# Kernel optimization log

Measured on AMD Instinct MI355X. Metric: run time of the kernel, lower is better.

The kernel has to match this reference:

```python
import jax, jax.numpy as jnp
import numpy as np
import math

_INV_SQRT2 = 1.0 / math.sqrt(2.0)
B, N, D, H = 4, 8192, 1024, 16
DH = D // H  # 64
GH = 4 * DH  # 256


def setup_inputs() -> dict:
    key = jax.random.key(0)
    ks = jax.random.split(key, 8)
    std = 0.02
    return {
        "x": jax.random.normal(ks[0], (B, N, D), jnp.float32),
        "w_q": jax.random.normal(ks[1], (D, D), jnp.float32) * std,
        "w_v": jax.random.normal(ks[2], (D, D), jnp.float32) * std,
        "w_o": jax.random.normal(ks[3], (D, D), jnp.float32) * std,
        "ln_g": jnp.ones((DH,), jnp.float32),
        "ln_b": jnp.zeros((DH,), jnp.float32),
        "gate_w1": jax.random.normal(ks[4], (DH, GH), jnp.float32) * std,
        "gate_w2": jax.random.normal(ks[5], (GH, 2 * N), jnp.float32) * std,
        "wrm_w1": jax.random.normal(ks[6], (DH, GH), jnp.float32) * std,
        "wrm_w2": jax.random.normal(ks[7], (GH, N), jnp.float32) * std,
    }


def reference(x, w_q, w_v, w_o, ln_g, ln_b, gate_w1, gate_w2, wrm_w1, wrm_w2):
    b, n, d = x.shape
    h, dh = H, DH
    # projections -> (b, h, n, dh)
    q = (x @ w_q).reshape(b, n, h, dh).transpose(0, 2, 1, 3)
    v = (x @ w_v).reshape(b, n, h, dh).transpose(0, 2, 1, 3)
    # per-head summary query + LayerNorm (biased variance, eps=1e-5)
    bar_q = q.mean(axis=2)  # (b, h, dh)
    mu = bar_q.mean(axis=-1, keepdims=True)
    var = ((bar_q - mu) ** 2).mean(axis=-1, keepdims=True)
    bar_q = (bar_q - mu) / jnp.sqrt(var + 1e-5) * ln_g + ln_b
    # complex spectral gate: (b, h, 2n) -> real || imag
    g_raw = jax.nn.gelu(bar_q @ gate_w1, approximate=False) @ gate_w2
    g = g_raw[..., :n] + 1j * g_raw[..., n:]  # (b, h, n) complex
    # FFT -> gate -> IFFT along sequence axis
    v_hat = jnp.fft.fft(v, axis=2) * g[..., None]
    v_tilde = jnp.fft.ifft(v_hat, axis=2).real.astype(x.dtype)
    # Haar wavelet refinement
    even, odd = v_tilde[..., 0::2, :], v_tilde[..., 1::2, :]
    w_hat = jnp.concatenate([(even + odd) * _INV_SQRT2,
                             (even - odd) * _INV_SQRT2], axis=-2)
    s = (jax.nn.gelu(bar_q @ wrm_w1, approximate=False) @ wrm_w2)[..., None]
    w_hat = w_hat * s
    half = n // 2
    low, high = w_hat[..., :half, :], w_hat[..., half:, :]
    ev = (low + high) * _INV_SQRT2
    od = (low - high) * _INV_SQRT2
    v_ref = jnp.stack([ev, od], axis=-2).reshape(b, h, n, dh)  # interleave even/odd
    v_tilde = v_tilde + v_ref
    y = v_tilde.transpose(0, 2, 1, 3).reshape(b, n, d)
    return y @ w_o
```

## Files before the change

kernel.cpp:

```cpp
#include <hip/hip_runtime.h>
#include <hip/hip_bf16.h>
#include <math.h>

#define PB 4
#define PN 8192
#define PD 1024
#define PH 16
#define PDH 64
#define PGH 256

typedef __bf16 bf16x8 __attribute__((ext_vector_type(8)));
typedef __bf16 bf16x2 __attribute__((ext_vector_type(2)));
typedef float f32x4 __attribute__((ext_vector_type(4)));
typedef unsigned int u32;
typedef unsigned short u16;

typedef __attribute__((address_space(3))) void lds_void_t;
typedef const __attribute__((address_space(1))) void gbl_void_t;
#define ASYNC_COPY16(gp, lp) \
    __builtin_amdgcn_global_load_lds((gbl_void_t*)(gp), (lds_void_t*)(lp), 16, 0, 0)

__device__ inline float gelu_exact(float x) {
    return 0.5f * x * (1.0f + erff(x * 0.70710678118654752440f));
}

__device__ inline float2 f2(float x, float y) { return make_float2(x, y); }
__device__ inline float2 cadd(float2 a, float2 b) { return f2(a.x + b.x, a.y + b.y); }
__device__ inline float2 csub(float2 a, float2 b) { return f2(a.x - b.x, a.y - b.y); }
__device__ inline float2 cmul(float2 a, float2 b) {
    return f2(a.x * b.x - a.y * b.y, a.x * b.y + a.y * b.x);
}

#define PHYS(i) ((i) ^ (((i) >> 4) & 15))

__device__ inline u32 packbf(float a, float b) {
    __bf16 ba = (__bf16)a, bb = (__bf16)b;
    return (u32)(*(u16*)&ba) | ((u32)(*(u16*)&bb) << 16);
}

__global__ void convert_x(const float* __restrict__ x, __bf16* __restrict__ xb) {
    int i = (blockIdx.x * 256 + threadIdx.x) * 8;
    float4 f0 = *(const float4*)(x + i);
    float4 f1 = *(const float4*)(x + i + 4);
    bf16x8 o;
    o[0] = (__bf16)f0.x; o[1] = (__bf16)f0.y; o[2] = (__bf16)f0.z; o[3] = (__bf16)f0.w;
    o[4] = (__bf16)f1.x; o[5] = (__bf16)f1.y; o[6] = (__bf16)f1.z; o[7] = (__bf16)f1.w;
    *(bf16x8*)(xb + i) = o;
}

__global__ void transpose_w(const float* __restrict__ wv, const float* __restrict__ wo,
                            __bf16* __restrict__ wvt, __bf16* __restrict__ wot) {
    int idx = blockIdx.x * 256 + threadIdx.x;
    const float* src = blockIdx.y ? wo : wv;
    __bf16* dst = blockIdx.y ? wot : wvt;
    int r = idx >> 10, c = idx & 1023;
    dst[c * PD + r] = (__bf16)src[idx];
}

__global__ void reduce_x(const float* __restrict__ x, float* __restrict__ xsum) {
    int b = blockIdx.z;
    int d = blockIdx.y * 256 + threadIdx.x;
    int n0 = blockIdx.x * 512;
    const float* p = x + ((size_t)b * PN + n0) * PD + d;
    float s = 0.0f;
    for (int i = 0; i < 512; i++) s += p[(size_t)i * PD];
    atomicAdd(&xsum[b * PD + d], s);
}

__global__ void barq_ln(const float* __restrict__ xsum, const float* __restrict__ w_q,
                        const float* __restrict__ ln_g, const float* __restrict__ ln_b,
                        float* __restrict__ bar_ln) {
    int b = blockIdx.y;
    int c = blockIdx.x * 256 + threadIdx.x;
    const float* xs = xsum + b * PD;
    float acc = 0.0f;
    for (int k = 0; k < PD; k++) acc += xs[k] * w_q[k * PD + c];
    float bar = acc * (1.0f / (float)PN);
    float mu = bar;
    for (int o = 32; o > 0; o >>= 1) mu += __shfl_xor(mu, o, 64);
    mu *= (1.0f / 64.0f);
    float d0 = bar - mu;
    float vv = d0 * d0;
    for (int o = 32; o > 0; o >>= 1) vv += __shfl_xor(vv, o, 64);
    vv *= (1.0f / 64.0f);
    int dh = c & 63;
    bar_ln[b * PD + c] = d0 * rsqrtf(vv + 1e-5f) * ln_g[dh] + ln_b[dh];
}

__global__ void small1(const float* __restrict__ bar_ln, const float* __restrict__ gw1,
                       const float* __restrict__ ww1, float* __restrict__ tg,
                       float* __restrict__ tw) {
    int bh = blockIdx.x;
    int j = threadIdx.x;
    __shared__ float bl[PDH];
    if (j < PDH) bl[j] = bar_ln[bh * PDH + j];
    __syncthreads();
    float a1 = 0.0f, a2 = 0.0f;
    for (int k = 0; k < PDH; k++) {
        float bv = bl[k];
        a1 += bv * gw1[k * PGH + j];
        a2 += bv * ww1[k * PGH + j];
    }
    tg[bh * PGH + j] = gelu_exact(a1);
    tw[bh * PGH + j] = gelu_exact(a2);
}

__global__ void small2(const float* __restrict__ tg, const float* __restrict__ tw,
                       const float* __restrict__ gw2, const float* __restrict__ ww2,
                       float* __restrict__ g_raw, float* __restrict__ s_full) {
    int chunk = blockIdx.x;
    int bh0 = blockIdx.y * 8;
    bool isg = chunk < 64;
    const float* t = isg ? tg : tw;
    const float* w2 = isg ? gw2 : ww2;
    int stride = isg ? (2 * PN) : PN;
    int col = (isg ? chunk : chunk - 64) * 256 + threadIdx.x;
    __shared__ float tl[8][PGH];
    #pragma unroll
    for (int i = 0; i < 8; i++) tl[i][threadIdx.x] = t[(bh0 + i) * PGH + threadIdx.x];
    __syncthreads();
    float acc[8] = {0, 0, 0, 0, 0, 0, 0, 0};
    for (int k = 0; k < PGH; k++) {
        float w = w2[(size_t)k * stride + col];
        #pragma unroll
        for (int i = 0; i < 8; i++) acc[i] += tl[i][k] * w;
    }
    #pragma unroll
    for (int i = 0; i < 8; i++) {
        if (isg) g_raw[(size_t)(bh0 + i) * (2 * PN) + col] = acc[i];
        else     s_full[(size_t)(bh0 + i) * PN + col] = acc[i];
    }
}

__global__ __launch_bounds__(256) void gemm_pair(const __bf16* __restrict__ A,
                                                 const __bf16* __restrict__ Bt,
                                                 u32* __restrict__ vt) {
    constexpr int K = PD, LDK = 32;
    __shared__ __attribute__((aligned(16))) __bf16 As[128 * LDK];
    __shared__ __attribute__((aligned(16))) __bf16 Bs[128 * LDK];
    const int tid = threadIdx.x;
    const int lane = tid & 63;
    const int wave = tid >> 6;
    const int wm = (wave >> 1) << 6;
    const int wn = (wave & 1) << 6;
    const int tileM = blockIdx.y << 7;
    const int tileN = blockIdx.x << 7;
    const int r = tid >> 2;
    const int cg = tid & 3;
    const int mrow = lane & 15;
    const int k0 = (lane >> 4) << 3;

    f32x4 acc[4][4] = {};
    const __bf16* Aptr = A + (size_t)(tileM + r) * K + cg * 8;
    const __bf16* Bptr = Bt + (size_t)(tileN + r) * K + cg * 8;

    for (int kt = 0; kt < K; kt += 32) {
        __syncthreads();
        ASYNC_COPY16(Aptr + kt,                  As + tid * 8);
        ASYNC_COPY16(Aptr + (size_t)64 * K + kt, As + 64 * LDK + tid * 8);
        ASYNC_COPY16(Bptr + kt,                  Bs + tid * 8);
        ASYNC_COPY16(Bptr + (size_t)64 * K + kt, Bs + 64 * LDK + tid * 8);
        __syncthreads();
        bf16x8 af[4], bfr[4];
        #pragma unroll
        for (int i = 0; i < 4; i++) af[i]  = *(const bf16x8*)&As[(wm + i * 16 + mrow) * LDK + k0];
        #pragma unroll
        for (int j = 0; j < 4; j++) bfr[j] = *(const bf16x8*)&Bs[(wn + j * 16 + mrow) * LDK + k0];
        #pragma unroll
        for (int i = 0; i < 4; i++)
            #pragma unroll
            for (int j = 0; j < 4; j++)
                acc[i][j] = __builtin_amdgcn_mfma_f32_16x16x32_bf16(af[i], bfr[j], acc[i][j], 0, 0, 0);
    }

    const int rq = (lane >> 4) << 2;
    const bool evl = (lane & 1) == 0;
    #pragma unroll
    for (int i = 0; i < 4; i++) {
        int grow = tileM + wm + i * 16 + rq;
        int b = grow >> 13;
        int nb = grow & 8191;
        #pragma unroll
        for (int j = 0; j < 4; j++) {
            u32 w[4];
            #pragma unroll
            for (int rr = 0; rr < 4; rr++) {
                float a = acc[i][j][rr];
                float o = __shfl_xor(a, 1, 64);
                w[rr] = packbf(a, o);
            }
            if (evl) {
                int col = tileN + wn + j * 16 + mrow;
                size_t idx = ((size_t)b * 512 + (col >> 1)) * PN + nb;
                *(uint4*)(vt + idx) = make_uint4(w[0], w[1], w[2], w[3]);
            }
        }
    }
}

__global__ __launch_bounds__(256) void gemm_ta(const u32* __restrict__ yt,
                                               const __bf16* __restrict__ Bt,
                                               float* __restrict__ Cf) {
    constexpr int K = PD, Nc = PD, LDKA = 40, LDKB = 32;
    __shared__ __attribute__((aligned(16))) __bf16 As[128 * LDKA];
    __shared__ __attribute__((aligned(16))) __bf16 Bs[128 * LDKB];
    u32* As32 = (u32*)As;
    const int tid = threadIdx.x;
    const int lane = tid & 63;
    const int wave = tid >> 6;
    const int wm = (wave >> 1) << 6;
    const int wn = (wave & 1) << 6;
    const int tileM = blockIdx.y << 7;
    const int tileN = blockIdx.x << 7;
    const int r = tid >> 2;
    const int cg = tid & 3;
    const int mrow = lane & 15;
    const int k0 = (lane >> 4) << 3;
    const int prow = tid & 7;
    const int seg = tid >> 3;

    const int b = tileM >> 13;
    const int n0 = tileM & 8191;
    const u32* abase = yt + ((size_t)b * 512 + prow) * PN + n0 + seg * 4;
    const __bf16* Bptr = Bt + (size_t)(tileN + r) * K + cg * 8;

    f32x4 acc[4][4] = {};
    uint4 pa0 = *(const uint4*)(abase);
    uint4 pa1 = *(const uint4*)(abase + (size_t)8 * PN);

    for (int kt = 0; kt < K; kt += 32) {
        __syncthreads();
        {
            int m0 = seg * 4;
            As32[(m0 + 0) * 20 + prow] = pa0.x;
            As32[(m0 + 1) * 20 + prow] = pa0.y;
            As32[(m0 + 2) * 20 + prow] = pa0.z;
            As32[(m0 + 3) * 20 + prow] = pa0.w;
            As32[(m0 + 0) * 20 + prow + 8] = pa1.x;
            As32[(m0 + 1) * 20 + prow + 8] = pa1.y;
            As32[(m0 + 2) * 20 + prow + 8] = pa1.z;
            As32[(m0 + 3) * 20 + prow + 8] = pa1.w;
        }
        ASYNC_COPY16(Bptr + kt,                  Bs + tid * 8);
        ASYNC_COPY16(Bptr + (size_t)64 * K + kt, Bs + 64 * LDKB + tid * 8);
        if (kt + 32 < K) {
            const u32* nxt = abase + (size_t)((kt >> 1) + 16) * PN;
            pa0 = *(const uint4*)(nxt);
            pa1 = *(const uint4*)(nxt + (size_t)8 * PN);
        }
        __syncthreads();
        bf16x8 af[4], bfr[4];
        #pragma unroll
        for (int i = 0; i < 4; i++) af[i]  = *(const bf16x8*)&As[(wm + i * 16 + mrow) * LDKA + k0];
        #pragma unroll
        for (int j = 0; j < 4; j++) bfr[j] = *(const bf16x8*)&Bs[(wn + j * 16 + mrow) * LDKB + k0];
        #pragma unroll
        for (int i = 0; i < 4; i++)
            #pragma unroll
            for (int j = 0; j < 4; j++)
                acc[i][j] = __builtin_amdgcn_mfma_f32_16x16x32_bf16(af[i], bfr[j], acc[i][j], 0, 0, 0);
    }

    const int rq = (lane >> 4) << 2;
    #pragma unroll
    for (int i = 0; i < 4; i++) {
        #pragma unroll
        for (int rr = 0; rr < 4; rr++) {
            int row = tileM + wm + i * 16 + rq + rr;
            size_t base = (size_t)row * Nc + tileN + wn + mrow;
            #pragma unroll
            for (int j = 0; j < 4; j++) Cf[base + j * 16] = acc[i][j][rr];
        }
    }
}

__global__ __launch_bounds__(512) void fftconv(const u32* __restrict__ vt,
                                               const float* __restrict__ g_raw,
                                               const float* __restrict__ s_full,
                                               u32* __restrict__ yt) {
    __shared__ float2 Z[PN];
    const int tid = threadIdx.x;
    const int row = blockIdx.x;
    const int bh = row >> 5;
    const u32* vp = vt + (size_t)row * PN;

    #pragma unroll
    for (int it = 0; it < 2; it++) {
        int n0 = (tid + it * 512) * 8;
        uint4 u0 = *(const uint4*)(vp + n0);
        uint4 u1 = *(const uint4*)(vp + n0 + 4);
        u32 uu[8] = {u0.x, u0.y, u0.z, u0.w, u1.x, u1.y, u1.z, u1.w};
        #pragma unroll
        for (int m = 0; m < 8; m++) {
            bf16x2 p = *(bf16x2*)&uu[m];
            Z[PHYS(n0 + m)] = f2((float)p.x, (float)p.y);
        }
    }
    __syncthreads();

    #pragma unroll
    for (int si = 0; si < 6; si++) {
        const int s = 11 - 2 * si;
        const int h = 1 << s;
        const float ang = -6.283185307179586f / (float)(4 * h);
        float sn, cs;
        __sincosf(ang * (float)(tid & (h - 1)), &sn, &cs);
        float2 w2 = f2(cs, sn);
        #pragma unroll
        for (int it = 0; it < 4; it++) {
            int q = tid + it * 512;
            int i = ((q >> s) << (s + 2)) + (q & (h - 1));
            float2 w1 = cmul(w2, w2);
            float2 a = Z[PHYS(i)],         bb = Z[PHYS(i + h)];
            float2 c = Z[PHYS(i + 2 * h)], d  = Z[PHYS(i + 3 * h)];
            float2 A0 = cadd(a, c);
            float2 C0 = cmul(csub(a, c), w2);
            float2 B0 = cadd(bb, d);
            float2 t  = cmul(csub(bb, d), w2);
            float2 D0 = f2(t.y, -t.x);
            Z[PHYS(i)]         = cadd(A0, B0);
            Z[PHYS(i + h)]     = cmul(csub(A0, B0), w1);
            Z[PHYS(i + 2 * h)] = cadd(C0, D0);
            Z[PHYS(i + 3 * h)] = cmul(csub(C0, D0), w1);
            if (h == 2048) w2 = cmul(w2, f2(0.92387953251f, -0.38268343236f));
        }
        __syncthreads();
    }
    #pragma unroll
    for (int it = 0; it < 8; it++) {
        int i = 2 * (tid + it * 512);
        float2 u = Z[PHYS(i)], t = Z[PHYS(i + 1)];
        Z[PHYS(i)]     = cadd(u, t);
        Z[PHYS(i + 1)] = csub(u, t);
    }
    __syncthreads();

    const float* gr = g_raw + (size_t)bh * (2 * PN);
    const float* gi = gr + PN;
    for (int m = tid; m < PN / 2 + 1; m += 512) {
        int p  = (m < PN / 2) ? 2 * m : 1;
        int k  = __brev((unsigned)p) >> 19;
        int Nk = (PN - k) & (PN - 1);
        int qd = __brev((unsigned)Nk) >> 19;
        float2 Za = Z[PHYS(p)], Zb = Z[PHYS(qd)];
        float v1r = 0.5f * (Za.x + Zb.x), v1i = 0.5f * (Za.y - Zb.y);
        float v2r = 0.5f * (Za.y + Zb.y), v2i = 0.5f * (Zb.x - Za.x);
        float grk = gr[k],  gik = gi[k];
        float grn = gr[Nk], gin = gi[Nk];
        float y1r  = v1r * grk - v1i * gik, y1i  = v1r * gik + v1i * grk;
        float y2r  = v2r * grk - v2i * gik, y2i  = v2r * gik + v2i * grk;
        float y1nr = v1r * grn + v1i * gin, y1ni = v1r * gin - v1i * grn;
        float y2nr = v2r * grn + v2i * gin, y2ni = v2r * gin - v2i * grn;
        float ys1r = 0.5f * (y1r + y1nr), ys1i = 0.5f * (y1i - y1ni);
        float ys2r = 0.5f * (y2r + y2nr), ys2i = 0.5f * (y2i - y2ni);
        Z[PHYS(p)] = f2(ys1r - ys2i, ys1i + ys2r);
        if (qd != p) Z[PHYS(qd)] = f2(ys1r + ys2i, ys2r - ys1i);
    }
    __syncthreads();

    #pragma unroll
    for (int si = 0; si < 6; si++) {
        const int s = 2 * si;
        const int h = 1 << s;
        const float ang = 6.283185307179586f / (float)(4 * h);
        float sn, cs;
        __sincosf(ang * (float)(tid & (h - 1)), &sn, &cs);
        float2 w2a = f2(cs, sn);
        float2 w2b = (h == 1024) ? cmul(w2a, f2(0.70710678119f, 0.70710678119f)) : w2a;
        #pragma unroll
        for (int it = 0; it < 4; it++) {
            int q = tid + it * 512;
            int i = ((q >> s) << (s + 2)) + (q & (h - 1));
            float2 w2 = (it & 1) ? w2b : w2a;
            float2 w1 = cmul(w2, w2);
            float2 a = Z[PHYS(i)],         bb = Z[PHYS(i + h)];
            float2 c = Z[PHYS(i + 2 * h)], d  = Z[PHYS(i + 3 * h)];
            float2 tb = cmul(bb, w1);
            float2 p0 = cadd(a, tb), p1 = csub(a, tb);
            float2 td = cmul(d, w1);
            float2 q0 = cadd(c, td), q1 = csub(c, td);
            float2 wq0 = cmul(q0, w2);
            float2 e   = cmul(q1, w2);
            float2 ei  = f2(-e.y, e.x);
            Z[PHYS(i)]         = cadd(p0, wq0);
            Z[PHYS(i + 2 * h)] = csub(p0, wq0);
            Z[PHYS(i + h)]     = cadd(p1, ei);
            Z[PHYS(i + 3 * h)] = csub(p1, ei);
        }
        __syncthreads();
    }
    {
        const float ang = 6.283185307179586f / (float)PN;
        float sn, cs;
        __sincosf(ang * (float)tid, &sn, &cs);
        float2 w = f2(cs, sn);
        #pragma unroll
        for (int it = 0; it < 8; it++) {
            int q = tid + it * 512;
            float2 u = Z[PHYS(q)];
            float2 t = cmul(Z[PHYS(q + PN / 2)], w);
            Z[PHYS(q)]          = cadd(u, t);
            Z[PHYS(q + PN / 2)] = csub(u, t);
            w = cmul(w, f2(0.92387953251f, 0.38268343236f));
        }
    }
    __syncthreads();

    const float* sp = s_full + (size_t)bh * PN;
    u32* yp = yt + (size_t)row * PN;
    const float inv = 1.0f / (float)PN;
    const float I2 = 0.70710678118654752440f;
    #pragma unroll
    for (int it = 0; it < 2; it++) {
        int nb = tid + it * 512;
        int n0 = nb * 8;
        int np0 = nb * 4;
        u32 ou[8];
        #pragma unroll
        for (int pp = 0; pp < 4; pp++) {
            float2 z0 = Z[PHYS(n0 + 2 * pp)];
            float2 z1 = Z[PHYS(n0 + 2 * pp + 1)];
            float s0  = sp[np0 + pp];
            float s1v = sp[np0 + pp + PN / 2];
            float ax = z0.x * inv, ay = z0.y * inv;
            float bx = z1.x * inv, by = z1.y * inv;
            float wlx = (ax + bx) * I2 * s0, whx = (ax - bx) * I2 * s1v;
            float evx = (wlx + whx) * I2,   odx = (wlx - whx) * I2;
            float wly = (ay + by) * I2 * s0, why = (ay - by) * I2 * s1v;
            float evy = (wly + why) * I2,   ody = (wly - why) * I2;
            ou[2 * pp]     = packbf(ax + evx, ay + evy);
            ou[2 * pp + 1] = packbf(bx + odx, by + ody);
        }
        *(uint4*)(yp + n0)     = make_uint4(ou[0], ou[1], ou[2], ou[3]);
        *(uint4*)(yp + n0 + 4) = make_uint4(ou[4], ou[5], ou[6], ou[7]);
    }
}

extern "C" void kernel_launch(void* const* d_in, const int* in_sizes, int n_in,
                              void* d_out, int out_size, void* d_ws, size_t ws_size,
                              hipStream_t stream) {
    const float* x    = (const float*)d_in[0];
    const float* w_q  = (const float*)d_in[1];
    const float* w_v  = (const float*)d_in[2];
    const float* w_o  = (const float*)d_in[3];
    const float* ln_g = (const float*)d_in[4];
    const float* ln_b = (const float*)d_in[5];
    const float* gw1  = (const float*)d_in[6];
    const float* gw2  = (const float*)d_in[7];
    const float* ww1  = (const float*)d_in[8];
    const float* ww2  = (const float*)d_in[9];
    float* out = (float*)d_out;

    const size_t XE = (size_t)PB * PN * PD;
    __bf16* xb   = (__bf16*)d_ws;
    __bf16* vb   = xb + XE;
    __bf16* wvt  = vb + XE;
    __bf16* wot  = wvt + (size_t)PD * PD;
    float*  xsum = (float*)(wot + (size_t)PD * PD);
    float*  bar  = xsum + PB * PD;
    float*  tg   = bar + PB * PD;
    float*  tw   = tg + 64 * PGH;
    float*  graw = tw + 64 * PGH;
    float*  sful = graw + (size_t)64 * 2 * PN;

    hipMemsetAsync(xsum, 0, PB * PD * sizeof(float), stream);

    convert_x<<<XE / (256 * 8), 256, 0, stream>>>(x, xb);
    transpose_w<<<dim3(PD * PD / 256, 2), 256, 0, stream>>>(w_v, w_o, wvt, wot);
    reduce_x<<<dim3(PN / 512, PD / 256, PB), 256, 0, stream>>>(x, xsum);
    barq_ln<<<dim3(PD / 256, PB), 256, 0, stream>>>(xsum, w_q, ln_g, ln_b, bar);
    small1<<<PB * PH, 256, 0, stream>>>(bar, gw1, ww1, tg, tw);
    small2<<<dim3(96, 8), 256, 0, stream>>>(tg, tw, gw2, ww2, graw, sful);
    gemm_pair<<<dim3(PD / 128, PB * PN / 128), 256, 0, stream>>>(xb, wvt, (u32*)vb);
    fftconv<<<PB * 512, 512, 0, stream>>>((const u32*)vb, graw, sful, (u32*)xb);
    gemm_ta<<<dim3(PD / 128, PB * PN / 128), 256, 0, stream>>>((const u32*)xb, wot, out);
}
```

Before: 779.1 us.

## Fuse x conversion with reduction, tile weight transpose, register-blocked radix-16 FFT

Result: faster. 724.8 us (-7.0%).

```diff
diff --git a/kernel.cpp b/kernel.cpp
--- a/kernel.cpp
+++ b/kernel.cpp
@@ -38,53 +38,150 @@
     return (u32)(*(u16*)&ba) | ((u32)(*(u16*)&bb) << 16);
 }
 
-__global__ void convert_x(const float* __restrict__ x, __bf16* __restrict__ xb) {
-    int i = (blockIdx.x * 256 + threadIdx.x) * 8;
-    float4 f0 = *(const float4*)(x + i);
-    float4 f1 = *(const float4*)(x + i + 4);
-    bf16x8 o;
-    o[0] = (__bf16)f0.x; o[1] = (__bf16)f0.y; o[2] = (__bf16)f0.z; o[3] = (__bf16)f0.w;
-    o[4] = (__bf16)f1.x; o[5] = (__bf16)f1.y; o[6] = (__bf16)f1.z; o[7] = (__bf16)f1.w;
-    *(bf16x8*)(xb + i) = o;
+__device__ inline void dif4(float2& a, float2& b, float2& c, float2& d,
+                            float2 w2, float2 w1) {
+    float2 A0 = cadd(a, c);
+    float2 C0 = cmul(csub(a, c), w2);
+    float2 B0 = cadd(b, d);
+    float2 t  = cmul(csub(b, d), w2);
+    float2 D0 = f2(t.y, -t.x);
+    a = cadd(A0, B0);
+    b = cmul(csub(A0, B0), w1);
+    c = cadd(C0, D0);
+    d = cmul(csub(C0, D0), w1);
+}
+
+__device__ inline void dit4(float2& a, float2& b, float2& c, float2& d,
+                            float2 w2, float2 w1) {
+    float2 tb = cmul(b, w1);
+    float2 p0 = cadd(a, tb), p1 = csub(a, tb);
+    float2 td = cmul(d, w1);
+    float2 q0 = cadd(c, td), q1 = csub(c, td);
+    float2 wq0 = cmul(q0, w2);
+    float2 e   = cmul(q1, w2);
+    float2 ei  = f2(-e.y, e.x);
+    a = cadd(p0, wq0);
+    c = csub(p0, wq0);
+    b = cadd(p1, ei);
+    d = csub(p1, ei);
+}
+
+template<int S>
+__device__ inline void fwd16_layers(float2 X[4][4], int u) {
+    const int h4 = 1 << (S - 2);
+    const int off = u & (h4 - 1);
+    float sn, cs;
+    const float ang1 = -6.283185307179586f / (float)(1 << (S + 2));
+    __sincosf(ang1 * (float)off, &sn, &cs);
+    float2 w2 = f2(cs, sn);
+    const float2 c8m = f2(0.92387953251129f, -0.38268343236509f);
+    #pragma unroll
+    for (int b = 0; b < 4; b++) {
+        float2 w1 = cmul(w2, w2);
+        dif4(X[0][b], X[1][b], X[2][b], X[3][b], w2, w1);
+        w2 = cmul(w2, c8m);
+    }
+    const float ang2 = -6.283185307179586f / (float)(1 << S);
+    __sincosf(ang2 * (float)off, &sn, &cs);
+    float2 v2 = f2(cs, sn);
+    float2 v1 = cmul(v2, v2);
+    #pragma unroll
+    for (int a = 0; a < 4; a++)
+        dif4(X[a][0], X[a][1], X[a][2], X[a][3], v2, v1);
+}
+
+template<int S>
+__device__ inline void inv16_layers(float2 X[4][4], int u) {
+    const int h = 1 << S;
+    const int off = u & (h - 1);
+    float sn, cs;
+    const float ang1 = 6.283185307179586f / (float)(4 * h);
+    __sincosf(ang1 * (float)off, &sn, &cs);
+    float2 w2 = f2(cs, sn), w1 = cmul(w2, w2);
+    #pragma unroll
+    for (int a = 0; a < 4; a++)
+        dit4(X[a][0], X[a][1], X[a][2], X[a][3], w2, w1);
+    const float ang2 = 6.283185307179586f / (float)(16 * h);
+    __sincosf(ang2 * (float)off, &sn, &cs);
+    float2 v2 = f2(cs, sn);
+    const float2 c8p = f2(0.92387953251129f, 0.38268343236509f);
+    #pragma unroll
+    for (int b = 0; b < 4; b++) {
+        float2 v1 = cmul(v2, v2);
+        dit4(X[0][b], X[1][b], X[2][b], X[3][b], v2, v1);
+        v2 = cmul(v2, c8p);
+    }
+}
+
+__device__ inline void r2_shfl(float2 X[4][4], bool ev) {
+    #pragma unroll
+    for (int a = 0; a < 4; a++)
+        #pragma unroll
+        for (int b = 0; b < 4; b++) {
+            float2 o = f2(__shfl_xor(X[a][b].x, 1, 64), __shfl_xor(X[a][b].y, 1, 64));
+            X[a][b] = ev ? cadd(X[a][b], o) : csub(o, X[a][b]);
+        }
+}
+
+__global__ void convert_reduce(const float* __restrict__ x, __bf16* __restrict__ xb,
+                               float* __restrict__ xsum) {
+    int b = blockIdx.z;
+    int d = blockIdx.y * 256 + threadIdx.x;
+    int n0 = blockIdx.x * 256;
+    const float* p = x + ((size_t)b * PN + n0) * PD + d;
+    __bf16* q = xb + ((size_t)b * PN + n0) * PD + d;
+    float s = 0.0f;
+    #pragma unroll 4
+    for (int i = 0; i < 256; i++) {
+        float v = p[(size_t)i * PD];
+        s += v;
+        q[(size_t)i * PD] = (__bf16)v;
+    }
+    atomicAdd(&xsum[b * PD + d], s);
 }
 
 __global__ void transpose_w(const float* __restrict__ wv, const float* __restrict__ wo,
                             __bf16* __restrict__ wvt, __bf16* __restrict__ wot) {
-    int idx = blockIdx.x * 256 + threadIdx.x;
-    const float* src = blockIdx.y ? wo : wv;
-    __bf16* dst = blockIdx.y ? wot : wvt;
-    int r = idx >> 10, c = idx & 1023;
-    dst[c * PD + r] = (__bf16)src[idx];
-}
-
-__global__ void reduce_x(const float* __restrict__ x, float* __restrict__ xsum) {
-    int b = blockIdx.z;
-    int d = blockIdx.y * 256 + threadIdx.x;
-    int n0 = blockIdx.x * 512;
-    const float* p = x + ((size_t)b * PN + n0) * PD + d;
-    float s = 0.0f;
-    for (int i = 0; i < 512; i++) s += p[(size_t)i * PD];
-    atomicAdd(&xsum[b * PD + d], s);
+    __shared__ float t[64][65];
+    const float* src = blockIdx.z ? wo : wv;
+    __bf16* dst = blockIdx.z ? wot : wvt;
+    int r0 = blockIdx.y * 64, c0 = blockIdx.x * 64;
+    int lr = threadIdx.x >> 6, lc = threadIdx.x & 63;
+    #pragma unroll
+    for (int i = 0; i < 16; i++)
+        t[lr + 4 * i][lc] = src[(size_t)(r0 + lr + 4 * i) * PD + c0 + lc];
+    __syncthreads();
+    #pragma unroll
+    for (int i = 0; i < 16; i++)
+        dst[(size_t)(c0 + lr + 4 * i) * PD + r0 + lc] = (__bf16)t[lc][lr + 4 * i];
 }
 
 __global__ void barq_ln(const float* __restrict__ xsum, const float* __restrict__ w_q,
                         const float* __restrict__ ln_g, const float* __restrict__ ln_b,
                         float* __restrict__ bar_ln) {
     int b = blockIdx.y;
-    int c = blockIdx.x * 256 + threadIdx.x;
-    const float* xs = xsum + b * PD;
+    int lane = threadIdx.x & 63;
+    int w = threadIdx.x >> 6;
+    int c = blockIdx.x * 64 + lane;
+    const float* xs = xsum + b * PD + w * 256;
+    const float* wq = w_q + (size_t)(w * 256) * PD + c;
     float acc = 0.0f;
-    for (int k = 0; k < PD; k++) acc += xs[k] * w_q[k * PD + c];
-    float bar = acc * (1.0f / (float)PN);
-    float mu = bar;
-    for (int o = 32; o > 0; o >>= 1) mu += __shfl_xor(mu, o, 64);
-    mu *= (1.0f / 64.0f);
-    float d0 = bar - mu;
-    float vv = d0 * d0;
-    for (int o = 32; o > 0; o >>= 1) vv += __shfl_xor(vv, o, 64);
-    vv *= (1.0f / 64.0f);
-    int dh = c & 63;
-    bar_ln[b * PD + c] = d0 * rsqrtf(vv + 1e-5f) * ln_g[dh] + ln_b[dh];
+    for (int k = 0; k < 256; k++) acc += xs[k] * wq[(size_t)k * PD];
+    __shared__ float part[4][64];
+    part[w][lane] = acc;
+    __syncthreads();
+    if (w == 0) {
+        float bar = (part[0][lane] + part[1][lane] + part[2][lane] + part[3][lane])
+                    * (1.0f / (float)PN);
+        float mu = bar;
+        for (int o = 32; o > 0; o >>= 1) mu += __shfl_xor(mu, o, 64);
+        mu *= (1.0f / 64.0f);
+        float d0 = bar - mu;
+        float vv = d0 * d0;
+        for (int o = 32; o > 0; o >>= 1) vv += __shfl_xor(vv, o, 64);
+        vv *= (1.0f / 64.0f);
+        bar_ln[b * PD + c] = d0 * rsqrtf(vv + 1e-5f) * ln_g[lane] + ln_b[lane];
+    }
 }
 
 __global__ void small1(const float* __restrict__ bar_ln, const float* __restrict__ gw1,
@@ -283,156 +380,167 @@
     const int row = blockIdx.x;
     const int bh = row >> 5;
     const u32* vp = vt + (size_t)row * PN;
-
-    #pragma unroll
-    for (int it = 0; it < 2; it++) {
-        int n0 = (tid + it * 512) * 8;
-        uint4 u0 = *(const uint4*)(vp + n0);
-        uint4 u1 = *(const uint4*)(vp + n0 + 4);
-        u32 uu[8] = {u0.x, u0.y, u0.z, u0.w, u1.x, u1.y, u1.z, u1.w};
-        #pragma unroll
-        for (int m = 0; m < 8; m++) {
-            bf16x2 p = *(bf16x2*)&uu[m];
-            Z[PHYS(n0 + m)] = f2((float)p.x, (float)p.y);
-        }
-    }
-    __syncthreads();
-
-    #pragma unroll
-    for (int si = 0; si < 6; si++) {
-        const int s = 11 - 2 * si;
-        const int h = 1 << s;
-        const float ang = -6.283185307179586f / (float)(4 * h);
-        float sn, cs;
-        __sincosf(ang * (float)(tid & (h - 1)), &sn, &cs);
-        float2 w2 = f2(cs, sn);
-        #pragma unroll
-        for (int it = 0; it < 4; it++) {
-            int q = tid + it * 512;
-            int i = ((q >> s) << (s + 2)) + (q & (h - 1));
-            float2 w1 = cmul(w2, w2);
-            float2 a = Z[PHYS(i)],         bb = Z[PHYS(i + h)];
-            float2 c = Z[PHYS(i + 2 * h)], d  = Z[PHYS(i + 3 * h)];
-            float2 A0 = cadd(a, c);
-            float2 C0 = cmul(csub(a, c), w2);
-            float2 B0 = cadd(bb, d);
-            float2 t  = cmul(csub(bb, d), w2);
-            float2 D0 = f2(t.y, -t.x);
-            Z[PHYS(i)]         = cadd(A0, B0);
-            Z[PHYS(i + h)]     = cmul(csub(A0, B0), w1);
-            Z[PHYS(i + 2 * h)] = cadd(C0, D0);
-            Z[PHYS(i + 3 * h)] = cmul(csub(C0, D0), w1);
-            if (h == 2048) w2 = cmul(w2, f2(0.92387953251f, -0.38268343236f));
-        }
-        __syncthreads();
-    }
-    #pragma unroll
-    for (int it = 0; it < 8; it++) {
-        int i = 2 * (tid + it * 512);
-        float2 u = Z[PHYS(i)], t = Z[PHYS(i + 1)];
-        Z[PHYS(i)]     = cadd(u, t);
-        Z[PHYS(i + 1)] = csub(u, t);
-    }
-    __syncthreads();
-
-    const float* gr = g_raw + (size_t)bh * (2 * PN);
-    const float* gi = gr + PN;
-    for (int m = tid; m < PN / 2 + 1; m += 512) {
-        int p  = (m < PN / 2) ? 2 * m : 1;
-        int k  = __brev((unsigned)p) >> 19;
-        int Nk = (PN - k) & (PN - 1);
-        int qd = __brev((unsigned)Nk) >> 19;
-        float2 Za = Z[PHYS(p)], Zb = Z[PHYS(qd)];
-        float v1r = 0.5f * (Za.x + Zb.x), v1i = 0.5f * (Za.y - Zb.y);
-        float v2r = 0.5f * (Za.y + Zb.y), v2i = 0.5f * (Zb.x - Za.x);
-        float grk = gr[k],  gik = gi[k];
-        float grn = gr[Nk], gin = gi[Nk];
-        float y1r  = v1r * grk - v1i * gik, y1i  = v1r * gik + v1i * grk;
-        float y2r  = v2r * grk - v2i * gik, y2i  = v2r * gik + v2i * grk;
-        float y1nr = v1r * grn + v1i * gin, y1ni = v1r * gin - v1i * grn;
-        float y2nr = v2r * grn + v2i * gin, y2ni = v2r * gin - v2i * grn;
-        float ys1r = 0.5f * (y1r + y1nr), ys1i = 0.5f * (y1i - y1ni);
-        float ys2r = 0.5f * (y2r + y2nr), ys2i = 0.5f * (y2i - y2ni);
-        Z[PHYS(p)] = f2(ys1r - ys2i, ys1i + ys2r);
-        if (qd != p) Z[PHYS(qd)] = f2(ys1r + ys2i, ys2r - ys1i);
-    }
-    __syncthreads();
-
-    #pragma unroll
-    for (int si = 0; si < 6; si++) {
-        const int s = 2 * si;
-        const int h = 1 << s;
-        const float ang = 6.283185307179586f / (float)(4 * h);
-        float sn, cs;
-        __sincosf(ang * (float)(tid & (h - 1)), &sn, &cs);
-        float2 w2a = f2(cs, sn);
-        float2 w2b = (h == 1024) ? cmul(w2a, f2(0.70710678119f, 0.70710678119f)) : w2a;
-        #pragma unroll
-        for (int it = 0; it < 4; it++) {
-            int q = tid + it * 512;
-            int i = ((q >> s) << (s + 2)) + (q & (h - 1));
-            float2 w2 = (it & 1) ? w2b : w2a;
-            float2 w1 = cmul(w2, w2);
-            float2 a = Z[PHYS(i)],         bb = Z[PHYS(i + h)];
-            float2 c = Z[PHYS(i + 2 * h)], d  = Z[PHYS(i + 3 * h)];
-            float2 tb = cmul(bb, w1);
-            float2 p0 = cadd(a, tb), p1 = csub(a, tb);
-            float2 td = cmul(d, w1);
-            float2 q0 = cadd(c, td), q1 = csub(c, td);
-            float2 wq0 = cmul(q0, w2);
-            float2 e   = cmul(q1, w2);
-            float2 ei  = f2(-e.y, e.x);
-            Z[PHYS(i)]         = cadd(p0, wq0);
-            Z[PHYS(i + 2 * h)] = csub(p0, wq0);
-            Z[PHYS(i + h)]     = cadd(p1, ei);
-            Z[PHYS(i + 3 * h)] = csub(p1, ei);
-        }
-        __syncthreads();
-    }
-    {
-        const float ang = 6.283185307179586f / (float)PN;
-        float sn, cs;
-        __sincosf(ang * (float)tid, &sn, &cs);
-        float2 w = f2(cs, sn);
-        #pragma unroll
-        for (int it = 0; it < 8; it++) {
-            int q = tid + it * 512;
-            float2 u = Z[PHYS(q)];
-            float2 t = cmul(Z[PHYS(q + PN / 2)], w);
-            Z[PHYS(q)]          = cadd(u, t);
-            Z[PHYS(q + PN / 2)] = csub(u, t);
-            w = cmul(w, f2(0.92387953251f, 0.38268343236f));
-        }
-    }
-    __syncthreads();
-
-    const float* sp = s_full + (size_t)bh * PN;
-    u32* yp = yt + (size_t)row * PN;
-    const float inv = 1.0f / (float)PN;
-    const float I2 = 0.70710678118654752440f;
-    #pragma unroll
-    for (int it = 0; it < 2; it++) {
-        int nb = tid + it * 512;
-        int n0 = nb * 8;
-        int np0 = nb * 4;
-        u32 ou[8];
-        #pragma unroll
-        for (int pp = 0; pp < 4; pp++) {
-            float2 z0 = Z[PHYS(n0 + 2 * pp)];
-            float2 z1 = Z[PHYS(n0 + 2 * pp + 1)];
-            float s0  = sp[np0 + pp];
-            float s1v = sp[np0 + pp + PN / 2];
-            float ax = z0.x * inv, ay = z0.y * inv;
-            float bx = z1.x * inv, by = z1.y * inv;
-            float wlx = (ax + bx) * I2 * s0, whx = (ax - bx) * I2 * s1v;
-            float evx = (wlx + whx) * I2,   odx = (wlx - whx) * I2;
-            float wly = (ay + by) * I2 * s0, why = (ay - by) * I2 * s1v;
-            float evy = (wly + why) * I2,   ody = (wly - why) * I2;
-            ou[2 * pp]     = packbf(ax + evx, ay + evy);
-            ou[2 * pp + 1] = packbf(bx + odx, by + ody);
-        }
-        *(uint4*)(yp + n0)     = make_uint4(ou[0], ou[1], ou[2], ou[3]);
-        *(uint4*)(yp + n0 + 4) = make_uint4(ou[4], ou[5], ou[6], ou[7]);
+    const bool ev = (tid & 1) == 0;
+
+    {
+        float2 X[4][4];
+        #pragma unroll
+        for (int a = 0; a < 4; a++)
+            #pragma unroll
+            for (int b = 0; b < 4; b++) {
+                u32 pw = vp[tid + a * 2048 + b * 512];
+                bf16x2 pp = *(bf16x2*)&pw;
+                X[a][b] = f2((float)pp.x, (float)pp.y);
+            }
+        fwd16_layers<11>(X, tid);
+        #pragma unroll
+        for (int a = 0; a < 4; a++)
+            #pragma unroll
+            for (int b = 0; b < 4; b++)
+                Z[PHYS(tid + a * 2048 + b * 512)] = X[a][b];
+    }
+    __syncthreads();
+
+    {
+        const int base = ((tid >> 5) << 9) + (tid & 31);
+        float2 X[4][4];
+        #pragma unroll
+        for (int a = 0; a < 4; a++)
+            #pragma unroll
+            for (int b = 0; b < 4; b++)
+                X[a][b] = Z[PHYS(base + a * 128 + b * 32)];
+        fwd16_layers<7>(X, tid);
+        #pragma unroll
+        for (int a = 0; a < 4; a++)
+            #pragma unroll
+            for (int b = 0; b < 4; b++)
+                Z[PHYS(base + a * 128 + b * 32)] = X[a][b];
+    }
+    __syncthreads();
+
+    {
+        const int base = ((tid >> 1) << 5) + (tid & 1);
+        float2 X[4][4];
+        #pragma unroll
+        for (int a = 0; a < 4; a++)
+            #pragma unroll
+            for (int b = 0; b < 4; b++)
+                X[a][b] = Z[PHYS(base + a * 8 + b * 2)];
+        fwd16_layers<3>(X, tid);
+        r2_shfl(X, ev);
+        #pragma unroll
+        for (int a = 0; a < 4; a++)
+            #pragma unroll
+            for (int b = 0; b < 4; b++)
+                Z[PHYS(base + a * 8 + b * 2)] = X[a][b];
+    }
+    __syncthreads();
+
+    {
+        const float* gr = g_raw + (size_t)bh * (2 * PN);
+        const float* gi = gr + PN;
+        for (int m = tid; m < PN / 2 + 1; m += 512) {
+            int p  = (m < PN / 2) ? 2 * m : 1;
+            int k  = __brev((unsigned)p) >> 19;
+            int Nk = (PN - k) & (PN - 1);
+            int qd = __brev((unsigned)Nk) >> 19;
+            float2 Za = Z[PHYS(p)], Zb = Z[PHYS(qd)];
+            float v1r = 0.5f * (Za.x + Zb.x), v1i = 0.5f * (Za.y - Zb.y);
+            float v2r = 0.5f * (Za.y + Zb.y), v2i = 0.5f * (Zb.x - Za.x);
+            float grk = gr[k],  gik = gi[k];
+            float grn = gr[Nk], gin = gi[Nk];
+            float y1r  = v1r * grk - v1i * gik, y1i  = v1r * gik + v1i * grk;
+            float y2r  = v2r * grk - v2i * gik, y2i  = v2r * gik + v2i * grk;
+            float y1nr = v1r * grn + v1i * gin, y1ni = v1r * gin - v1i * grn;
+            float y2nr = v2r * grn + v2i * gin, y2ni = v2r * gin - v2i * grn;
+            float ys1r = 0.5f * (y1r + y1nr), ys1i = 0.5f * (y1i - y1ni);
+            float ys2r = 0.5f * (y2r + y2nr), ys2i = 0.5f * (y2i - y2ni);
+            Z[PHYS(p)] = f2(ys1r - ys2i, ys1i + ys2r);
+            if (qd != p) Z[PHYS(qd)] = f2(ys1r + ys2i, ys2r - ys1i);
+        }
+    }
+    __syncthreads();
+
+    {
+        const int base = ((tid >> 1) << 5) + (tid & 1);
+        float2 X[4][4];
+        #pragma unroll
+        for (int a = 0; a < 4; a++)
+            #pragma unroll
+            for (int b = 0; b < 4; b++)
+                X[a][b] = Z[PHYS(base + a * 8 + b * 2)];
+        r2_shfl(X, ev);
+        inv16_layers<1>(X, tid);
+        #pragma unroll
+        for (int a = 0; a < 4; a++)
+            #pragma unroll
+            for (int b = 0; b < 4; b++)
+                Z[PHYS(base + a * 8 + b * 2)] = X[a][b];
+    }
+    __syncthreads();
+
+    {
+        const int base = ((tid >> 5) << 9) + (tid & 31);
+        float2 X[4][4];
+        #pragma unroll
+        for (int a = 0; a < 4; a++)
+            #pragma unroll
+            for (int b = 0; b < 4; b++)
+                X[a][b] = Z[PHYS(base + a * 128 + b * 32)];
+        inv16_layers<5>(X, tid);
+        #pragma unroll
+        for (int a = 0; a < 4; a++)
+            #pragma unroll
+            for (int b = 0; b < 4; b++)
+                Z[PHYS(base + a * 128 + b * 32)] = X[a][b];
+    }
+    __syncthreads();
+
+    {
+        float2 X[4][4];
+        #pragma unroll
+        for (int a = 0; a < 4; a++)
+            #pragma unroll
+            for (int b = 0; b < 4; b++)
+                X[a][b] = Z[PHYS(tid + a * 2048 + b * 512)];
+        inv16_layers<9>(X, tid);
+        #pragma unroll
+        for (int a = 0; a < 4; a++)
+            #pragma unroll
+            for (int b = 0; b < 4; b++)
+                Z[PHYS(tid + a * 2048 + b * 512)] = X[a][b];
+    }
+    __syncthreads();
+
+    {
+        const float* sp = s_full + (size_t)bh * PN;
+        u32* yp = yt + (size_t)row * PN;
+        const float inv = 1.0f / (float)PN;
+        const float I2 = 0.70710678118654752440f;
+        #pragma unroll
+        for (int it = 0; it < 2; it++) {
+            int nb = tid + it * 512;
+            int n0 = nb * 8;
+            int np0 = nb * 4;
+            u32 ou[8];
+            #pragma unroll
+            for (int pp = 0; pp < 4; pp++) {
+                float2 z0 = Z[PHYS(n0 + 2 * pp)];
+                float2 z1 = Z[PHYS(n0 + 2 * pp + 1)];
+                float s0  = sp[np0 + pp];
+                float s1v = sp[np0 + pp + PN / 2];
+                float ax = z0.x * inv, ay = z0.y * inv;
+                float bx = z1.x * inv, by = z1.y * inv;
+                float wlx = (ax + bx) * I2 * s0, whx = (ax - bx) * I2 * s1v;
+                float evx = (wlx + whx) * I2,   odx = (wlx - whx) * I2;
+                float wly = (ay + by) * I2 * s0, why = (ay - by) * I2 * s1v;
+                float evy = (wly + why) * I2,   ody = (wly - why) * I2;
+                ou[2 * pp]     = packbf(ax + evx, ay + evy);
+                ou[2 * pp + 1] = packbf(bx + odx, by + ody);
+            }
+            *(uint4*)(yp + n0)     = make_uint4(ou[0], ou[1], ou[2], ou[3]);
+            *(uint4*)(yp + n0 + 4) = make_uint4(ou[4], ou[5], ou[6], ou[7]);
+        }
     }
 }
 
@@ -465,10 +573,9 @@
 
     hipMemsetAsync(xsum, 0, PB * PD * sizeof(float), stream);
 
-    convert_x<<<XE / (256 * 8), 256, 0, stream>>>(x, xb);
-    transpose_w<<<dim3(PD * PD / 256, 2), 256, 0, stream>>>(w_v, w_o, wvt, wot);
-    reduce_x<<<dim3(PN / 512, PD / 256, PB), 256, 0, stream>>>(x, xsum);
-    barq_ln<<<dim3(PD / 256, PB), 256, 0, stream>>>(xsum, w_q, ln_g, ln_b, bar);
+    convert_reduce<<<dim3(PN / 256, PD / 256, PB), 256, 0, stream>>>(x, xb, xsum);
+    transpose_w<<<dim3(16, 16, 2), 256, 0, stream>>>(w_v, w_o, wvt, wot);
+    barq_ln<<<dim3(PD / 64, PB), 256, 0, stream>>>(xsum, w_q, ln_g, ln_b, bar);
     small1<<<PB * PH, 256, 0, stream>>>(bar, gw1, ww1, tg, tw);
     small2<<<dim3(96, 8), 256, 0, stream>>>(tg, tw, gw2, ww2, graw, sful);
     gemm_pair<<<dim3(PD / 128, PB * PN / 128), 256, 0, stream>>>(xb, wvt, (u32*)vb);
```

## Fuse x conversion with column reduction, tile weight transpose, split barq, XCD-swizzle GEMMs

Applied to the files above, without the earlier changes.

Result: faster. 679.9 us (-12.7%).

```diff
diff --git a/kernel.cpp b/kernel.cpp
--- a/kernel.cpp
+++ b/kernel.cpp
@@ -38,53 +38,65 @@
     return (u32)(*(u16*)&ba) | ((u32)(*(u16*)&bb) << 16);
 }
 
-__global__ void convert_x(const float* __restrict__ x, __bf16* __restrict__ xb) {
-    int i = (blockIdx.x * 256 + threadIdx.x) * 8;
-    float4 f0 = *(const float4*)(x + i);
-    float4 f1 = *(const float4*)(x + i + 4);
-    bf16x8 o;
-    o[0] = (__bf16)f0.x; o[1] = (__bf16)f0.y; o[2] = (__bf16)f0.z; o[3] = (__bf16)f0.w;
-    o[4] = (__bf16)f1.x; o[5] = (__bf16)f1.y; o[6] = (__bf16)f1.z; o[7] = (__bf16)f1.w;
-    *(bf16x8*)(xb + i) = o;
+__global__ void convert_reduce(const float* __restrict__ x, __bf16* __restrict__ xb,
+                               float* __restrict__ xsum) {
+    int b = blockIdx.z;
+    int d = blockIdx.y * 256 + threadIdx.x;
+    int n0 = blockIdx.x * 256;
+    const float* p = x + ((size_t)b * PN + n0) * PD + d;
+    __bf16* q = xb + ((size_t)b * PN + n0) * PD + d;
+    float s = 0.0f;
+    #pragma unroll 4
+    for (int i = 0; i < 256; i++) {
+        float v = p[(size_t)i * PD];
+        s += v;
+        q[(size_t)i * PD] = (__bf16)v;
+    }
+    atomicAdd(&xsum[b * PD + d], s);
 }
 
 __global__ void transpose_w(const float* __restrict__ wv, const float* __restrict__ wo,
                             __bf16* __restrict__ wvt, __bf16* __restrict__ wot) {
-    int idx = blockIdx.x * 256 + threadIdx.x;
-    const float* src = blockIdx.y ? wo : wv;
-    __bf16* dst = blockIdx.y ? wot : wvt;
-    int r = idx >> 10, c = idx & 1023;
-    dst[c * PD + r] = (__bf16)src[idx];
-}
-
-__global__ void reduce_x(const float* __restrict__ x, float* __restrict__ xsum) {
-    int b = blockIdx.z;
-    int d = blockIdx.y * 256 + threadIdx.x;
-    int n0 = blockIdx.x * 512;
-    const float* p = x + ((size_t)b * PN + n0) * PD + d;
-    float s = 0.0f;
-    for (int i = 0; i < 512; i++) s += p[(size_t)i * PD];
-    atomicAdd(&xsum[b * PD + d], s);
+    __shared__ float t[64][65];
+    const float* src = blockIdx.z ? wo : wv;
+    __bf16* dst = blockIdx.z ? wot : wvt;
+    int r0 = blockIdx.y * 64, c0 = blockIdx.x * 64;
+    int lr = threadIdx.x >> 6, lc = threadIdx.x & 63;
+    #pragma unroll
+    for (int i = 0; i < 16; i++)
+        t[lr + 4 * i][lc] = src[(size_t)(r0 + lr + 4 * i) * PD + c0 + lc];
+    __syncthreads();
+    #pragma unroll
+    for (int i = 0; i < 16; i++)
+        dst[(size_t)(c0 + lr + 4 * i) * PD + r0 + lc] = (__bf16)t[lc][lr + 4 * i];
 }
 
 __global__ void barq_ln(const float* __restrict__ xsum, const float* __restrict__ w_q,
                         const float* __restrict__ ln_g, const float* __restrict__ ln_b,
                         float* __restrict__ bar_ln) {
     int b = blockIdx.y;
-    int c = blockIdx.x * 256 + threadIdx.x;
-    const float* xs = xsum + b * PD;
+    int lane = threadIdx.x & 63;
+    int w = threadIdx.x >> 6;
+    int c = blockIdx.x * 64 + lane;
+    const float* xs = xsum + b * PD + w * 256;
+    const float* wq = w_q + (size_t)(w * 256) * PD + c;
     float acc = 0.0f;
-    for (int k = 0; k < PD; k++) acc += xs[k] * w_q[k * PD + c];
-    float bar = acc * (1.0f / (float)PN);
-    float mu = bar;
-    for (int o = 32; o > 0; o >>= 1) mu += __shfl_xor(mu, o, 64);
-    mu *= (1.0f / 64.0f);
-    float d0 = bar - mu;
-    float vv = d0 * d0;
-    for (int o = 32; o > 0; o >>= 1) vv += __shfl_xor(vv, o, 64);
-    vv *= (1.0f / 64.0f);
-    int dh = c & 63;
-    bar_ln[b * PD + c] = d0 * rsqrtf(vv + 1e-5f) * ln_g[dh] + ln_b[dh];
+    for (int k = 0; k < 256; k++) acc += xs[k] * wq[(size_t)k * PD];
+    __shared__ float part[4][64];
+    part[w][lane] = acc;
+    __syncthreads();
+    if (w == 0) {
+        float bar = (part[0][lane] + part[1][lane] + part[2][lane] + part[3][lane])
+                    * (1.0f / (float)PN);
+        float mu = bar;
+        for (int o = 32; o > 0; o >>= 1) mu += __shfl_xor(mu, o, 64);
+        mu *= (1.0f / 64.0f);
+        float d0 = bar - mu;
+        float vv = d0 * d0;
+        for (int o = 32; o > 0; o >>= 1) vv += __shfl_xor(vv, o, 64);
+        vv *= (1.0f / 64.0f);
+        bar_ln[b * PD + c] = d0 * rsqrtf(vv + 1e-5f) * ln_g[lane] + ln_b[lane];
+    }
 }
 
 __global__ void small1(const float* __restrict__ bar_ln, const float* __restrict__ gw1,
@@ -132,6 +144,16 @@
     }
 }
 
+__device__ inline void xcd_swizzle(int& tileM, int& tileN) {
+    int lin = blockIdx.x + (blockIdx.y << 3);
+    int xcd = lin & 7;
+    int idx = lin >> 3;
+    int yy = (xcd << 5) + (idx >> 3);
+    int xx = idx & 7;
+    tileM = yy << 7;
+    tileN = xx << 7;
+}
+
 __global__ __launch_bounds__(256) void gemm_pair(const __bf16* __restrict__ A,
                                                  const __bf16* __restrict__ Bt,
                                                  u32* __restrict__ vt) {
@@ -143,8 +165,8 @@
     const int wave = tid >> 6;
     const int wm = (wave >> 1) << 6;
     const int wn = (wave & 1) << 6;
-    const int tileM = blockIdx.y << 7;
-    const int tileN = blockIdx.x << 7;
+    int tileM, tileN;
+    xcd_swizzle(tileM, tileN);
     const int r = tid >> 2;
     const int cg = tid & 3;
     const int mrow = lane & 15;
@@ -210,8 +232,8 @@
     const int wave = tid >> 6;
     const int wm = (wave >> 1) << 6;
     const int wn = (wave & 1) << 6;
-    const int tileM = blockIdx.y << 7;
-    const int tileN = blockIdx.x << 7;
+    int tileM, tileN;
+    xcd_swizzle(tileM, tileN);
     const int r = tid >> 2;
     const int cg = tid & 3;
     const int mrow = lane & 15;
@@ -465,10 +487,9 @@
 
     hipMemsetAsync(xsum, 0, PB * PD * sizeof(float), stream);
 
-    convert_x<<<XE / (256 * 8), 256, 0, stream>>>(x, xb);
-    transpose_w<<<dim3(PD * PD / 256, 2), 256, 0, stream>>>(w_v, w_o, wvt, wot);
-    reduce_x<<<dim3(PN / 512, PD / 256, PB), 256, 0, stream>>>(x, xsum);
-    barq_ln<<<dim3(PD / 256, PB), 256, 0, stream>>>(xsum, w_q, ln_g, ln_b, bar);
+    convert_reduce<<<dim3(PN / 256, PD / 256, PB), 256, 0, stream>>>(x, xb, xsum);
+    transpose_w<<<dim3(16, 16, 2), 256, 0, stream>>>(w_v, w_o, wvt, wot);
+    barq_ln<<<dim3(PD / 64, PB), 256, 0, stream>>>(xsum, w_q, ln_g, ln_b, bar);
     small1<<<PB * PH, 256, 0, stream>>>(bar, gw1, ww1, tg, tw);
     small2<<<dim3(96, 8), 256, 0, stream>>>(tg, tw, gw2, ww2, graw, sful);
     gemm_pair<<<dim3(PD / 128, PB * PN / 128), 256, 0, stream>>>(xb, wvt, (u32*)vb);
```
